# Performance work log

Hardware: AMD Instinct MI355X
Metric: run time of the kernel (lower is better)

## Reference

```python
import jax, jax.numpy as jnp
import numpy as np

N_, E_, A_, B_, H_, DH_ = 8000, 12000, 48000, 64, 64, 4096
STEPS, POOL_ITERS = 4, 3

def rbf(x, K, cutoff):
    mu = jnp.linspace(0.0, cutoff, K).astype(x.dtype)
    gamma = 1.0 / (cutoff / (K - 1)) ** 2
    return jnp.exp(-gamma * (x[..., None] - mu) ** 2)

def gru_step(x, h, Wih, Whh, bih, bhh):
    gi = x @ Wih.T + bih
    gh = h @ Whh.T + bhh
    ir, iz, inew = jnp.split(gi, 3, axis=-1)
    hr, hz, hnew = jnp.split(gh, 3, axis=-1)
    r = jax.nn.sigmoid(ir + hr)
    z = jax.nn.sigmoid(iz + hz)
    n = jnp.tanh(inew + r * hnew)
    return (1.0 - z) * n + z * h

def lstm_step(x, h, c, Wih, Whh, bih, bhh):
    g = x @ Wih.T + bih + h @ Whh.T + bhh
    i, f, gg, o = jnp.split(g, 4, axis=-1)
    c2 = jax.nn.sigmoid(f) * c + jax.nn.sigmoid(i) * jnp.tanh(gg)
    h2 = jax.nn.sigmoid(o) * jnp.tanh(c2)
    return h2, c2

def seg_softmax(e, seg, num_seg):
    m = jax.ops.segment_max(e, seg, num_segments=num_seg)
    ex = jnp.exp(e - m[seg])
    s = jax.ops.segment_sum(ex, seg, num_segments=num_seg)
    return ex / s[seg]

def _forward(node_attribute, edge_attribute, edge_length, angle, edge_src, edge_dst, angle_src, angle_dst, graph_ids, projW, projb, bondW, bondb, efW, efb, gnn_b, buW, bub, auW, aub, gWih, gWhh, gbih, gbhh, sWih0, sWhh0, sbih0, sbhh0, sWih1, sWhh1, sbih1, sbhh1, spW, spb, prelu_a):
    N, E = node_attribute.shape[0], edge_src.shape[0]
    x0 = jax.nn.relu(node_attribute @ projW + projb)  # [N, H]
    len_rbf = rbf(edge_length, 8, 4.0)                # [E, 8]
    edge_feat = jnp.concatenate([edge_attribute, len_rbf], axis=-1)  # [E, 16]
    ee_feat = jnp.concatenate([rbf(angle, 8, float(np.pi)), len_rbf[angle_src]], axis=-1)  # [A, 16]
    Wb = (edge_feat @ bondW + bondb).reshape(E, H_, H_)  # per-bond weight matrices (constant over steps)
    Wa = (ee_feat @ efW + efb).reshape(-1, H_, H_)       # per-angle weight matrices
    nf, hid = x0, x0
    for _ in range(STEPS):
        bm = nf[edge_src]                                # gather src node feats per bond [E, H]
        ha = jax.nn.relu(bm @ auW + aub)                 # angle_update
        m_ang = jnp.einsum('ai,aio->ao', ha[angle_src], Wa)  # [A, H]
        amsg = jax.ops.segment_sum(m_ang, angle_dst, num_segments=E)  # scatter-sum to bonds
        hb = jax.nn.relu(bm @ buW + bub) + amsg          # bond_update + angle message
        m = jnp.einsum('ei,eio->eo', hb, Wb)             # [E, H]
        nf = jax.nn.relu(jax.ops.segment_sum(m, edge_dst, num_segments=N) + gnn_b)
        nf = gru_step(nf, hid, gWih, gWhh, gbih, gbhh)   # 1-step, 1-layer GRU: output == new hidden
        hid = nf
    agg = jnp.concatenate([nf, x0], axis=-1)             # [N, 2H]
    D = agg.shape[-1]
    q_star = jnp.zeros((B_, 2 * D), agg.dtype)
    h0 = jnp.zeros((B_, D), agg.dtype); c0 = h0
    h1 = h0; c1 = h0
    for _ in range(POOL_ITERS):                          # Set2Set
        h0, c0 = lstm_step(q_star, h0, c0, sWih0, sWhh0, sbih0, sbhh0)
        h1, c1 = lstm_step(h0, h1, c1, sWih1, sWhh1, sbih1, sbhh1)
        q = h1                                           # [B, D]
        e = jnp.sum(agg * q[graph_ids], axis=-1)         # [N]
        alpha = seg_softmax(e, graph_ids, B_)
        readout = jax.ops.segment_sum(alpha[:, None] * agg, graph_ids, num_segments=B_)
        q_star = jnp.concatenate([q, readout], axis=-1)  # [B, 2D]
    out = q_star @ spW + spb                             # [B, DH]
    return jnp.where(out >= 0, out, prelu_a * out)       # PReLU

def setup_inputs():
    key = jax.random.key(0)
    ks = jax.random.split(key, 40)
    r = lambda i, shape, s=1.0: s * jax.random.normal(ks[i], shape, jnp.float32)
    inp = {}
    inp['node_attribute'] = r(0, (N_, 110))
    inp['edge_attribute'] = r(1, (E_, 8))
    inp['edge_length'] = jax.random.uniform(ks[2], (E_,), jnp.float32, 0.5, 4.0)
    inp['angle'] = jax.random.uniform(ks[3], (A_,), jnp.float32, 0.0, float(np.pi))
    inp['edge_src'] = jax.random.randint(ks[4], (E_,), 0, N_)
    inp['edge_dst'] = jax.random.randint(ks[5], (E_,), 0, N_)
    inp['angle_src'] = jax.random.randint(ks[6], (A_,), 0, E_)
    inp['angle_dst'] = jax.random.randint(ks[7], (A_,), 0, E_)
    inp['graph_ids'] = jnp.sort(jax.random.randint(ks[8], (N_,), 0, B_))
    w = 0.05
    inp['projW'] = r(9, (110, H_), w); inp['projb'] = jnp.zeros((H_,), jnp.float32)
    inp['bondW'] = r(10, (16, H_ * H_), w); inp['bondb'] = jnp.zeros((H_ * H_,), jnp.float32)
    inp['efW'] = r(11, (16, H_ * H_), w); inp['efb'] = jnp.zeros((H_ * H_,), jnp.float32)
    inp['gnn_b'] = jnp.zeros((H_,), jnp.float32)
    inp['buW'] = r(12, (H_, H_), w); inp['bub'] = jnp.zeros((H_,), jnp.float32)
    inp['auW'] = r(13, (H_, H_), w); inp['aub'] = jnp.zeros((H_,), jnp.float32)
    inp['gWih'] = r(14, (3 * H_, H_), w); inp['gWhh'] = r(15, (3 * H_, H_), w)
    inp['gbih'] = jnp.zeros((3 * H_,), jnp.float32); inp['gbhh'] = jnp.zeros((3 * H_,), jnp.float32)
    D = 2 * H_  # Set2Set feature dim = 128
    inp['sWih0'] = r(16, (4 * D, 2 * D), w); inp['sWhh0'] = r(17, (4 * D, D), w)
    inp['sbih0'] = jnp.zeros((4 * D,), jnp.float32); inp['sbhh0'] = jnp.zeros((4 * D,), jnp.float32)
    inp['sWih1'] = r(18, (4 * D, D), w); inp['sWhh1'] = r(19, (4 * D, D), w)
    inp['sbih1'] = jnp.zeros((4 * D,), jnp.float32); inp['sbhh1'] = jnp.zeros((4 * D,), jnp.float32)
    inp['spW'] = r(20, (4 * H_, DH_), w); inp['spb'] = jnp.zeros((DH_,), jnp.float32)
    inp['prelu_a'] = jnp.full((1,), 0.25, jnp.float32)
    return inp

def reference(node_attribute, edge_attribute, edge_length, angle, edge_src, edge_dst, angle_src, angle_dst, graph_ids, projW, projb, bondW, bondb, efW, efb, gnn_b, buW, bub, auW, aub, gWih, gWhh, gbih, gbhh, sWih0, sWhh0, sbih0, sbhh0, sWih1, sWhh1, sbih1, sbhh1, spW, spb, prelu_a):
    return _forward(node_attribute, edge_attribute, edge_length, angle, edge_src, edge_dst, angle_src, angle_dst, graph_ids, projW, projb, bondW, bondb, efW, efb, gnn_b, buW, bub, auW, aub, gWih, gWhh, gbih, gbhh, sWih0, sWhh0, sbih0, sbhh0, sWih1, sWhh1, sbih1, sbhh1, spW, spb, prelu_a)
```

## Files before the change

kernel.cpp:

```cpp
#include <hip/hip_runtime.h>
#include <math.h>

#define N_N 8000
#define N_E 12000
#define N_A 48000
#define N_B 64
#define N_H 64
#define N_DH 4096

typedef _Float16 h16;
typedef __attribute__((ext_vector_type(8))) _Float16 h16x8;
typedef __attribute__((ext_vector_type(4))) float f32x4;

__device__ __forceinline__ float atomAddF(float* p, float v) {
  return __hip_atomic_fetch_add(p, v, __ATOMIC_RELAXED, __HIP_MEMORY_SCOPE_AGENT);
}
__device__ __forceinline__ float sigm(float x) { return 1.f / (1.f + expf(-x)); }

#define SB_PROJ 2000
#define SB_FEAT (SB_PROJ + 47)
#define SB_PREP (SB_FEAT + 1984)
#define SB_BND  (SB_PREP + 32)
#define SB_END  (SB_BND + 1250)
#define PREP_B0 32768
#define PREP_B1 (PREP_B0 + 69632)
#define PREP_B2 (PREP_B1 + 69632)
#define PREP_B3 (PREP_B2 + 4096)
#define PREP_B4 (PREP_B3 + 4096)
#define PREP_B5 (PREP_B4 + 131072)
#define PREP_B6 (PREP_B5 + 65536)
#define PREP_B7 (PREP_B6 + 65536)
#define PREP_B8 (PREP_B7 + 65536)

__global__ __launch_bounds__(256) void k_setup(
    const float* __restrict__ na, const float* __restrict__ projW,
    const float* __restrict__ projb, const float* __restrict__ ea,
    const float* __restrict__ el, const int* __restrict__ gid,
    const float* __restrict__ gWih, const float* __restrict__ gWhh,
    const float* __restrict__ efW, const float* __restrict__ efb,
    const float* __restrict__ bondW, const float* __restrict__ bondb,
    const float* __restrict__ auW, const float* __restrict__ buW,
    const float* __restrict__ sWih0, const float* __restrict__ sWhh0,
    const float* __restrict__ sWih1, const float* __restrict__ sWhh1,
    float* __restrict__ x0, float* __restrict__ ef,
    int* __restrict__ gstart, int* __restrict__ gend,
    h16* __restrict__ W3t, h16* __restrict__ ttA, h16* __restrict__ ttB,
    h16* __restrict__ wtAU, h16* __restrict__ wtBU,
    float* __restrict__ w0xT, float* __restrict__ w0hT,
    float* __restrict__ w1xT, float* __restrict__ w1hT,
    float4* __restrict__ amsg0_4, float4* __restrict__ nacc0_4) {
  int bx = blockIdx.x, tid = threadIdx.x;
  if (bx < SB_PROJ) {
    int wid = bx * 4 + (tid >> 6);
    int lane = tid & 63;
    if (wid < N_N) {
      const float* row = na + (size_t)wid * 110;
      float acc = projb[lane];
      for (int k = 0; k < 110; ++k) acc = fmaf(row[k], projW[k * 64 + lane], acc);
      x0[(size_t)wid * 64 + lane] = fmaxf(acc, 0.f);
    }
  } else if (bx < SB_FEAT) {
    int e = (bx - SB_PROJ) * 256 + tid;
    if (e < N_E) {
      const float g2 = (7.f / 4.f) * (7.f / 4.f);
      float x = el[e];
#pragma unroll
      for (int j = 0; j < 8; ++j) ef[e * 16 + j] = ea[e * 8 + j];
#pragma unroll
      for (int j = 0; j < 8; ++j) {
        float d = x - j * (4.f / 7.f);
        ef[e * 16 + 8 + j] = expf(-g2 * d * d);
      }
    }
  } else if (bx < SB_PREP) {
    int i = (bx - SB_FEAT) * 256 + tid;
    if (i < PREP_B0) {
      int col = i >> 7, k = i & 127;
      int grp = col >> 6, u = col & 63;
      float v;
      if (grp == 0) v = (k < 64) ? gWih[u * 64 + k] : gWhh[u * 64 + k - 64];
      else if (grp == 1) v = (k < 64) ? gWih[(64 + u) * 64 + k] : gWhh[(64 + u) * 64 + k - 64];
      else if (grp == 2) v = (k < 64) ? gWih[(128 + u) * 64 + k] : 0.f;
      else v = (k < 64) ? 0.f : gWhh[(128 + u) * 64 + k - 64];
      W3t[i] = (h16)v;
    } else if (i < PREP_B1) {
      int j = i - PREP_B0;
      int n = j >> 6, i2 = j & 63;
      int k = n >> 6, o = n & 63;
      float val = (k < 16) ? efW[(size_t)k * 4096 + i2 * 64 + o] : efb[i2 * 64 + o];
      ttA[j] = (h16)val;
    } else if (i < PREP_B2) {
      int j = i - PREP_B1;
      int n = j >> 6, i2 = j & 63;
      int k = n >> 6, o = n & 63;
      float val = (k < 16) ? bondW[(size_t)k * 4096 + i2 * 64 + o] : bondb[i2 * 64 + o];
      ttB[j] = (h16)val;
    } else if (i < PREP_B3) {
      int j = i - PREP_B2;
      int o = j >> 6, i2 = j & 63;
      wtAU[j] = (h16)auW[i2 * 64 + o];
    } else if (i < PREP_B4) {
      int j = i - PREP_B3;
      int o = j >> 6, i2 = j & 63;
      wtBU[j] = (h16)buW[i2 * 64 + o];
    } else if (i < PREP_B5) {
      int j = i - PREP_B4;
      int k = j >> 9, r = j & 511;
      w0xT[j] = sWih0[(size_t)r * 256 + k];
    } else if (i < PREP_B6) {
      int j = i - PREP_B5;
      int k = j >> 9, r = j & 511;
      w0hT[j] = sWhh0[(size_t)r * 128 + k];
    } else if (i < PREP_B7) {
      int j = i - PREP_B6;
      int k = j >> 9, r = j & 511;
      w1xT[j] = sWih1[(size_t)r * 128 + k];
    } else if (i < PREP_B8) {
      int j = i - PREP_B7;
      int k = j >> 9, r = j & 511;
      w1hT[j] = sWhh1[(size_t)r * 128 + k];
    }
  } else if (bx < SB_BND) {
    int n = (bx - SB_PREP) * 256 + tid;
    if (n < N_N) {
      int g = gid[n];
      if (n == 0 || gid[n - 1] != g) gstart[g] = n;
      if (n == N_N - 1 || gid[n + 1] != g) gend[g] = n + 1;
    }
  } else if (bx < SB_END) {
    int i = (bx - SB_BND) * 256 + tid;
    float4 z = (float4){0.f, 0.f, 0.f, 0.f};
    if (i < 192000) amsg0_4[i] = z;
    else if (i < 320000) nacc0_4[i - 192000] = z;
  }
}

__global__ __launch_bounds__(256) void k_edgeP(
    const float* __restrict__ xcur, const int* __restrict__ esrc,
    const h16* __restrict__ wtAU, const float* __restrict__ aub,
    const h16* __restrict__ ttA, const float* __restrict__ ef,
    h16* __restrict__ P8, float* __restrict__ Q) {
  __shared__ h16 haT[4][2048];
  __shared__ float f_lds[128 * 9];
  int tid = threadIdx.x, wave = tid >> 6, lane = tid & 63;
  int l15 = lane & 15, lq = lane >> 4;
  int oc = blockIdx.y;
  int base = blockIdx.x * 128;
  if (oc >= 2) {
    for (int e2 = tid; e2 < 128 * 8; e2 += 256) {
      int il = e2 >> 3, k = e2 & 7;
      int g = base + il;
      if (g >= N_E) g = N_E - 1;
      f_lds[il * 9 + k] = ef[(size_t)g * 16 + 8 + k];
    }
    __syncthreads();
  }
  int ibl = wave * 32, ib0 = base + ibl;
  h16* myT = haT[wave];

  {
    h16x8 xafr[2][2];
#pragma unroll
    for (int s = 0; s < 2; ++s) {
      int item = ib0 + s * 16 + l15;
      if (item >= N_E) item = N_E - 1;
      const float* vp = xcur + (size_t)esrc[item] * 64;
#pragma unroll
      for (int ks = 0; ks < 2; ++ks) {
        const float4* p = (const float4*)(vp + ks * 32 + 8 * lq);
        float4 v0 = p[0], v1 = p[1];
        h16x8 a;
        a[0] = (h16)v0.x; a[1] = (h16)v0.y; a[2] = (h16)v0.z; a[3] = (h16)v0.w;
        a[4] = (h16)v1.x; a[5] = (h16)v1.y; a[6] = (h16)v1.z; a[7] = (h16)v1.w;
        xafr[s][ks] = a;
      }
    }
    f32x4 aU[2][4];
#pragma unroll
    for (int s = 0; s < 2; ++s)
#pragma unroll
      for (int nt = 0; nt < 4; ++nt) aU[s][nt] = (f32x4){0.f, 0.f, 0.f, 0.f};
#pragma unroll
    for (int nt = 0; nt < 4; ++nt)
#pragma unroll
      for (int ks = 0; ks < 2; ++ks) {
        h16x8 b = *(const h16x8*)(wtAU + (size_t)(nt * 16 + l15) * 64 + ks * 32 + 8 * lq);
#pragma unroll
        for (int s = 0; s < 2; ++s)
          aU[s][nt] = __builtin_amdgcn_mfma_f32_16x16x32_f16(xafr[s][ks], b, aU[s][nt], 0, 0, 0);
      }
#pragma unroll
    for (int s = 0; s < 2; ++s)
#pragma unroll
      for (int nt = 0; nt < 4; ++nt) {
        int o = nt * 16 + l15;
        float bo = aub[o];
#pragma unroll
        for (int r = 0; r < 4; ++r) {
          int row = s * 16 + lq * 4 + r;
          float val = fmaxf(aU[s][nt][r] + bo, 0.f);
          int idx = (((row * 64 + o) << 1) ^ ((row & 7) << 4)) >> 1;
          myT[idx] = (h16)val;
        }
      }
  }
  h16x8 afr[2][2];
#pragma unroll
  for (int s = 0; s < 2; ++s)
#pragma unroll
    for (int ks = 0; ks < 2; ++ks) {
      int row = s * 16 + l15;
      int byte = ((row * 64 + ks * 32 + 8 * lq) << 1) ^ ((row & 7) << 4);
      afr[s][ks] = *(const h16x8*)((const char*)myT + byte);
    }

  if (oc < 2) {
#pragma unroll
    for (int kk = oc * 4; kk < oc * 4 + 4; ++kk) {
      f32x4 acc[2][4];
#pragma unroll
      for (int s = 0; s < 2; ++s)
#pragma unroll
        for (int nt = 0; nt < 4; ++nt) acc[s][nt] = (f32x4){0.f, 0.f, 0.f, 0.f};
#pragma unroll
      for (int nt = 0; nt < 4; ++nt)
#pragma unroll
        for (int ks = 0; ks < 2; ++ks) {
          h16x8 b = *(const h16x8*)(ttA + (size_t)(kk * 64 + nt * 16 + l15) * 64 +
                                    ks * 32 + 8 * lq);
#pragma unroll
          for (int s = 0; s < 2; ++s)
            acc[s][nt] = __builtin_amdgcn_mfma_f32_16x16x32_f16(afr[s][ks], b, acc[s][nt], 0, 0, 0);
        }
#pragma unroll
      for (int s = 0; s < 2; ++s)
#pragma unroll
        for (int r = 0; r < 4; ++r) {
          int e = ib0 + s * 16 + lq * 4 + r;
          if (e < N_E) {
#pragma unroll
            for (int nt = 0; nt < 4; ++nt)
              P8[((size_t)e * 8 + kk) * 64 + nt * 16 + l15] = (h16)acc[s][nt][r];
          }
        }
    }
  } else {
    int no = oc - 2;
    f32x4 qacc[2][2];
#pragma unroll
    for (int s = 0; s < 2; ++s)
#pragma unroll
      for (int nt = 0; nt < 2; ++nt) qacc[s][nt] = (f32x4){0.f, 0.f, 0.f, 0.f};
    for (int kk = 8; kk < 16; ++kk) {
      h16x8 a2[2][2];
#pragma unroll
      for (int s = 0; s < 2; ++s) {
        h16 fs = (h16)f_lds[(ibl + s * 16 + l15) * 9 + (kk - 8)];
        a2[s][0] = afr[s][0] * fs;
        a2[s][1] = afr[s][1] * fs;
      }
#pragma unroll
      for (int nt = 0; nt < 2; ++nt)
#pragma unroll
        for (int ks = 0; ks < 2; ++ks) {
          h16x8 b = *(const h16x8*)(ttA + (size_t)(kk * 64 + (no * 2 + nt) * 16 + l15) * 64 +
                                    ks * 32 + 8 * lq);
#pragma unroll
          for (int s = 0; s < 2; ++s)
            qacc[s][nt] = __builtin_amdgcn_mfma_f32_16x16x32_f16(a2[s][ks], b, qacc[s][nt], 0, 0, 0);
        }
    }
#pragma unroll
    for (int nt = 0; nt < 2; ++nt)
#pragma unroll
      for (int ks = 0; ks < 2; ++ks) {
        h16x8 b = *(const h16x8*)(ttA + (size_t)(16 * 64 + (no * 2 + nt) * 16 + l15) * 64 +
                                  ks * 32 + 8 * lq);
#pragma unroll
        for (int s = 0; s < 2; ++s)
          qacc[s][nt] = __builtin_amdgcn_mfma_f32_16x16x32_f16(afr[s][ks], b, qacc[s][nt], 0, 0, 0);
      }
#pragma unroll
    for (int s = 0; s < 2; ++s)
#pragma unroll
      for (int r = 0; r < 4; ++r) {
        int e = ib0 + s * 16 + lq * 4 + r;
        if (e < N_E) {
#pragma unroll
          for (int nt = 0; nt < 2; ++nt)
            Q[(size_t)e * 64 + (no * 2 + nt) * 16 + l15] = qacc[s][nt][r];
        }
      }
  }
}

__global__ __launch_bounds__(256) void k_angle(
    const float* __restrict__ ang, const int* __restrict__ asrc,
    const int* __restrict__ adst, const h16* __restrict__ P8,
    const float* __restrict__ Q, float* __restrict__ amsg) {
  int w = (blockIdx.x * blockDim.x + threadIdx.x) >> 6;
  int lane = threadIdx.x & 63;
  if (w >= N_A) return;
  float x = ang[w];
  int e = asrc[w], d = adst[w];
  float acc = Q[(size_t)e * 64 + lane];
  const h16* p = P8 + (size_t)e * 512;
  const float PIf = 3.14159265358979323846f;
  const float g1 = (7.f / PIf) * (7.f / PIf);
#pragma unroll
  for (int j = 0; j < 8; ++j) {
    float dd = x - j * (PIf / 7.f);
    acc = fmaf(expf(-g1 * dd * dd), (float)p[j * 64 + lane], acc);
  }
  atomAddF(amsg + (size_t)d * 64 + lane, acc);
}

__global__ __launch_bounds__(256) void k_bond(
    const float* __restrict__ xcur, const int* __restrict__ esrc,
    const h16* __restrict__ wtBU, const float* __restrict__ bub,
    const float* __restrict__ amsg_in, const float* __restrict__ ef,
    const h16* __restrict__ ttB, const int* __restrict__ edst,
    float* __restrict__ nacc, float4* __restrict__ zbuf, int zcount4) {
  if (blockIdx.y == 0) {
    int stride = gridDim.x * 256;
    for (int i = blockIdx.x * 256 + threadIdx.x; i < zcount4; i += stride)
      zbuf[i] = (float4){0.f, 0.f, 0.f, 0.f};
  }
  __shared__ h16 haT[4][2048];
  __shared__ float f_lds[128 * 17];
  __shared__ int dst_lds[128];
  int tid = threadIdx.x;
  int base = blockIdx.x * 128;
  int oc = blockIdx.y;
  for (int e2 = tid; e2 < 128 * 16; e2 += 256) {
    int il = e2 >> 4, k = e2 & 15;
    int g = base + il;
    if (g >= N_E) g = N_E - 1;
    f_lds[il * 17 + k] = ef[(size_t)g * 16 + k];
  }
  if (tid < 128) {
    int g = base + tid;
    if (g >= N_E) g = N_E - 1;
    dst_lds[tid] = edst[g];
  }
  __syncthreads();

  int wave = tid >> 6, lane = tid & 63;
  int l15 = lane & 15, lq = lane >> 4;
  int ibl = wave * 32, ib0 = base + ibl;
  h16* myT = haT[wave];

  {
    h16x8 xafr[2][2];
#pragma unroll
    for (int s = 0; s < 2; ++s) {
      int item = ib0 + s * 16 + l15;
      if (item >= N_E) item = N_E - 1;
      const float* vp = xcur + (size_t)esrc[item] * 64;
#pragma unroll
      for (int ks = 0; ks < 2; ++ks) {
        const float4* p = (const float4*)(vp + ks * 32 + 8 * lq);
        float4 v0 = p[0], v1 = p[1];
        h16x8 a;
        a[0] = (h16)v0.x; a[1] = (h16)v0.y; a[2] = (h16)v0.z; a[3] = (h16)v0.w;
        a[4] = (h16)v1.x; a[5] = (h16)v1.y; a[6] = (h16)v1.z; a[7] = (h16)v1.w;
        xafr[s][ks] = a;
      }
    }
    f32x4 aU[2][4];
#pragma unroll
    for (int s = 0; s < 2; ++s)
#pragma unroll
      for (int nt = 0; nt < 4; ++nt) aU[s][nt] = (f32x4){0.f, 0.f, 0.f, 0.f};
#pragma unroll
    for (int nt = 0; nt < 4; ++nt)
#pragma unroll
      for (int ks = 0; ks < 2; ++ks) {
        h16x8 b = *(const h16x8*)(wtBU + (size_t)(nt * 16 + l15) * 64 + ks * 32 + 8 * lq);
#pragma unroll
        for (int s = 0; s < 2; ++s)
          aU[s][nt] = __builtin_amdgcn_mfma_f32_16x16x32_f16(xafr[s][ks], b, aU[s][nt], 0, 0, 0);
      }
#pragma unroll
    for (int s = 0; s < 2; ++s)
#pragma unroll
      for (int nt = 0; nt < 4; ++nt) {
        int o = nt * 16 + l15;
        float bo = bub[o];
#pragma unroll
        for (int r = 0; r < 4; ++r) {
          int row = s * 16 + lq * 4 + r;
          int item = ib0 + row;
          if (item >= N_E) item = N_E - 1;
          float val = fmaxf(aU[s][nt][r] + bo, 0.f) + amsg_in[(size_t)item * 64 + o];
          int idx = (((row * 64 + o) << 1) ^ ((row & 7) << 4)) >> 1;
          myT[idx] = (h16)val;
        }
      }
  }
  h16x8 afr[2][2];
#pragma unroll
  for (int s = 0; s < 2; ++s)
#pragma unroll
    for (int ks = 0; ks < 2; ++ks) {
      int row = s * 16 + l15;
      int byte = ((row * 64 + ks * 32 + 8 * lq) << 1) ^ ((row & 7) << 4);
      afr[s][ks] = *(const h16x8*)((const char*)myT + byte);
    }

  f32x4 acc[2];
  acc[0] = (f32x4){0.f, 0.f, 0.f, 0.f};
  acc[1] = (f32x4){0.f, 0.f, 0.f, 0.f};
  for (int kk = 0; kk < 16; ++kk) {
    h16x8 bfr[2];
#pragma unroll
    for (int ks = 0; ks < 2; ++ks)
      bfr[ks] = *(const h16x8*)(ttB + (size_t)(kk * 64 + oc * 16 + l15) * 64 + ks * 32 + 8 * lq);
    h16x8 a2[2][2];
#pragma unroll
    for (int s = 0; s < 2; ++s) {
      h16 fs = (h16)f_lds[(ibl + s * 16 + l15) * 17 + kk];
      a2[s][0] = afr[s][0] * fs;
      a2[s][1] = afr[s][1] * fs;
    }
#pragma unroll
    for (int s = 0; s < 2; ++s)
#pragma unroll
      for (int ks = 0; ks < 2; ++ks)
        acc[s] = __builtin_amdgcn_mfma_f32_16x16x32_f16(a2[s][ks], bfr[ks], acc[s], 0, 0, 0);
  }
  {
    h16x8 bfr[2];
#pragma unroll
    for (int ks = 0; ks < 2; ++ks)
      bfr[ks] = *(const h16x8*)(ttB + (size_t)(16 * 64 + oc * 16 + l15) * 64 + ks * 32 + 8 * lq);
#pragma unroll
    for (int s = 0; s < 2; ++s)
#pragma unroll
      for (int ks = 0; ks < 2; ++ks)
        acc[s] = __builtin_amdgcn_mfma_f32_16x16x32_f16(afr[s][ks], bfr[ks], acc[s], 0, 0, 0);
  }
#pragma unroll
  for (int s = 0; s < 2; ++s)
#pragma unroll
    for (int r = 0; r < 4; ++r) {
      int il = ibl + s * 16 + lq * 4 + r;
      int item = base + il;
      if (item < N_E)
        atomAddF(nacc + (size_t)dst_lds[il] * 64 + oc * 16 + l15, acc[s][r]);
    }
}

__global__ __launch_bounds__(256) void k_gru2(
    const float* __restrict__ nacc, const float* __restrict__ gnnb,
    const float* __restrict__ h, const h16* __restrict__ W3t,
    const float* __restrict__ gbih, const float* __restrict__ gbhh,
    float* __restrict__ hout, const float* __restrict__ x0,
    float* __restrict__ agg, int wagg, float4* __restrict__ zbuf, int zcount4) {
  if (zbuf) {
    int stride = gridDim.x * 256;
    for (int i = blockIdx.x * 256 + threadIdx.x; i < zcount4; i += stride)
      zbuf[i] = (float4){0.f, 0.f, 0.f, 0.f};
  }
  int tid = threadIdx.x, wave = tid >> 6, lane = tid & 63;
  int l15 = lane & 15, lq = lane >> 4;
  int ib0 = blockIdx.x * 64 + wave * 16;
  int nodeA = ib0 + l15;
  if (nodeA >= N_N) nodeA = N_N - 1;

  h16x8 afr[4];
#pragma unroll
  for (int ks = 0; ks < 2; ++ks) {
    const float4* p = (const float4*)(nacc + (size_t)nodeA * 64 + ks * 32 + 8 * lq);
    const float4* gp = (const float4*)(gnnb + ks * 32 + 8 * lq);
    float4 v0 = p[0], v1 = p[1], g0 = gp[0], g1 = gp[1];
    h16x8 a;
    a[0] = (h16)fmaxf(v0.x + g0.x, 0.f); a[1] = (h16)fmaxf(v0.y + g0.y, 0.f);
    a[2] = (h16)fmaxf(v0.z + g0.z, 0.f); a[3] = (h16)fmaxf(v0.w + g0.w, 0.f);
    a[4] = (h16)fmaxf(v1.x + g1.x, 0.f); a[5] = (h16)fmaxf(v1.y + g1.y, 0.f);
    a[6] = (h16)fmaxf(v1.z + g1.z, 0.f); a[7] = (h16)fmaxf(v1.w + g1.w, 0.f);
    afr[ks] = a;
  }
#pragma unroll
  for (int ks = 0; ks < 2; ++ks) {
    const float4* p = (const float4*)(h + (size_t)nodeA * 64 + ks * 32 + 8 * lq);
    float4 v0 = p[0], v1 = p[1];
    h16x8 a;
    a[0] = (h16)v0.x; a[1] = (h16)v0.y; a[2] = (h16)v0.z; a[3] = (h16)v0.w;
    a[4] = (h16)v1.x; a[5] = (h16)v1.y; a[6] = (h16)v1.z; a[7] = (h16)v1.w;
    afr[2 + ks] = a;
  }

  f32x4 acc[16];
#pragma unroll
  for (int nt = 0; nt < 16; ++nt) acc[nt] = (f32x4){0.f, 0.f, 0.f, 0.f};
#pragma unroll
  for (int nt = 0; nt < 16; ++nt) {
#pragma unroll
    for (int ks = 0; ks < 4; ++ks) {
      if (nt >= 8 && nt < 12 && ks >= 2) continue;
      if (nt >= 12 && ks < 2) continue;
      h16x8 b = *(const h16x8*)(W3t + (size_t)(nt * 16 + l15) * 128 + ks * 32 + 8 * lq);
      acc[nt] = __builtin_amdgcn_mfma_f32_16x16x32_f16(afr[ks], b, acc[nt], 0, 0, 0);
    }
  }

#pragma unroll
  for (int nt0 = 0; nt0 < 4; ++nt0) {
    int u = nt0 * 16 + l15;
    float br = gbih[u] + gbhh[u];
    float bz = gbih[64 + u] + gbhh[64 + u];
    float bin_ = gbih[128 + u];
    float bhn = gbhh[128 + u];
#pragma unroll
    for (int r = 0; r < 4; ++r) {
      int node = ib0 + lq * 4 + r;
      if (node < N_N) {
        float rr = sigm(acc[nt0][r] + br);
        float zz = sigm(acc[nt0 + 4][r] + bz);
        float nn = tanhf(acc[nt0 + 8][r] + bin_ + rr * (acc[nt0 + 12][r] + bhn));
        float hv = h[(size_t)node * 64 + u];
        float val = (1.f - zz) * nn + zz * hv;
        hout[(size_t)node * 64 + u] = val;
        if (wagg) {
          agg[(size_t)node * 128 + u] = val;
          agg[(size_t)node * 128 + 64 + u] = x0[(size_t)node * 64 + u];
        }
      }
    }
  }
}

__global__ __launch_bounds__(256) void k_s2s(
    const float* __restrict__ agg, const int* __restrict__ gstart,
    const int* __restrict__ gend,
    const float* __restrict__ w0xT, const float* __restrict__ w0hT,
    const float* __restrict__ sbih0, const float* __restrict__ sbhh0,
    const float* __restrict__ w1xT, const float* __restrict__ w1hT,
    const float* __restrict__ sbih1, const float* __restrict__ sbhh1,
    const float* __restrict__ spW, const float* __restrict__ spb,
    const float* __restrict__ pa, float* __restrict__ out) {
  int g = blockIdx.x, tid = threadIdx.x;
  __shared__ float qs[256];
  __shared__ float h0[128], c0[128], h1[128], c1[128];
  __shared__ float gates[512];
  __shared__ float ew[1024];
  __shared__ float red[8];
  __shared__ float comb[256];
  if (tid < 256) qs[tid] = 0.f;
  if (tid < 128) { h0[tid] = 0.f; c0[tid] = 0.f; h1[tid] = 0.f; c1[tid] = 0.f; }
  int s = gstart[g], t = gend[g];
  int cnt = t - s;
  if (cnt < 0) cnt = 0;
  if (cnt > 1024) cnt = 1024;
  int wave = tid >> 6, lane = tid & 63;
  __syncthreads();

  for (int it = 0; it < 3; ++it) {
    {
      int r0 = tid, r1 = tid + 256;
      float a0 = sbih0[r0] + sbhh0[r0];
      float a1 = sbih0[r1] + sbhh0[r1];
      for (int k = 0; k < 256; ++k) {
        float xv = qs[k];
        a0 = fmaf(xv, w0xT[(size_t)k * 512 + r0], a0);
        a1 = fmaf(xv, w0xT[(size_t)k * 512 + r1], a1);
      }
      for (int k = 0; k < 128; ++k) {
        float hv = h0[k];
        a0 = fmaf(hv, w0hT[(size_t)k * 512 + r0], a0);
        a1 = fmaf(hv, w0hT[(size_t)k * 512 + r1], a1);
      }
      gates[r0] = a0;
      gates[r1] = a1;
    }
    __syncthreads();
    if (tid < 128) {
      float gi = gates[tid], gf = gates[128 + tid], gg = gates[256 + tid], go = gates[384 + tid];
      float c2 = sigm(gf) * c0[tid] + sigm(gi) * tanhf(gg);
      c0[tid] = c2;
      h0[tid] = sigm(go) * tanhf(c2);
    }
    __syncthreads();
    {
      int r0 = tid, r1 = tid + 256;
      float a0 = sbih1[r0] + sbhh1[r0];
      float a1 = sbih1[r1] + sbhh1[r1];
      for (int k = 0; k < 128; ++k) {
        float xv = h0[k], hv = h1[k];
        a0 = fmaf(xv, w1xT[(size_t)k * 512 + r0], a0);
        a1 = fmaf(xv, w1xT[(size_t)k * 512 + r1], a1);
        a0 = fmaf(hv, w1hT[(size_t)k * 512 + r0], a0);
        a1 = fmaf(hv, w1hT[(size_t)k * 512 + r1], a1);
      }
      gates[r0] = a0;
      gates[r1] = a1;
    }
    __syncthreads();
    if (tid < 128) {
      float gi = gates[tid], gf = gates[128 + tid], gg = gates[256 + tid], go = gates[384 + tid];
      float c2 = sigm(gf) * c1[tid] + sigm(gi) * tanhf(gg);
      c1[tid] = c2;
      h1[tid] = sigm(go) * tanhf(c2);
    }
    __syncthreads();
    for (int i = wave; i < cnt; i += 4) {
      int n = s + i;
      float a = agg[(size_t)n * 128 + lane] * h1[lane] +
                agg[(size_t)n * 128 + 64 + lane] * h1[64 + lane];
#pragma unroll
      for (int m = 1; m < 64; m <<= 1) a += __shfl_xor(a, m);
      if (lane == 0) ew[i] = a;
    }
    __syncthreads();
    float mx = -INFINITY;
    for (int i = tid; i < cnt; i += 256) mx = fmaxf(mx, ew[i]);
#pragma unroll
    for (int m = 1; m < 64; m <<= 1) mx = fmaxf(mx, __shfl_xor(mx, m));
    if (lane == 0) red[wave] = mx;
    __syncthreads();
    mx = fmaxf(fmaxf(red[0], red[1]), fmaxf(red[2], red[3]));
    float sm = 0.f;
    for (int i = tid; i < cnt; i += 256) sm += expf(ew[i] - mx);
#pragma unroll
    for (int m = 1; m < 64; m <<= 1) sm += __shfl_xor(sm, m);
    if (lane == 0) red[4 + wave] = sm;
    __syncthreads();
    sm = red[4] + red[5] + red[6] + red[7];
    float inv = (sm > 0.f) ? 1.f / sm : 0.f;
    __syncthreads();
    for (int i = tid; i < cnt; i += 256) ew[i] = expf(ew[i] - mx) * inv;
    __syncthreads();
    int d = tid & 127, half = tid >> 7;
    float acc = 0.f;
    for (int i = half; i < cnt; i += 2)
      acc = fmaf(ew[i], agg[(size_t)(s + i) * 128 + d], acc);
    comb[tid] = acc;
    __syncthreads();
    if (half == 0) {
      qs[d] = h1[d];
      qs[128 + d] = acc + comb[128 + tid];
    }
    __syncthreads();
  }
  float a_ = pa[0];
  float oacc[16];
#pragma unroll
  for (int j = 0; j < 16; ++j) oacc[j] = spb[j * 256 + tid];
  for (int k = 0; k < 256; ++k) {
    float qv = qs[k];
    const float* wr = spW + (size_t)k * 4096;
#pragma unroll
    for (int j = 0; j < 16; ++j) oacc[j] = fmaf(qv, wr[j * 256 + tid], oacc[j]);
  }
#pragma unroll
  for (int j = 0; j < 16; ++j) {
    float v = oacc[j];
    out[(size_t)g * 4096 + j * 256 + tid] = v >= 0.f ? v : a_ * v;
  }
}

enum : size_t {
  OFF_X0 = 0,
  OFF_HA = OFF_X0 + (size_t)N_N * 64,
  OFF_HB = OFF_HA + (size_t)N_N * 64,
  OFF_EF = OFF_HB + (size_t)N_N * 64,
  OFF_AMSG0 = OFF_EF + (size_t)N_E * 16,
  OFF_AMSG1 = OFF_AMSG0 + (size_t)N_E * 64,
  OFF_NACC0 = OFF_AMSG1 + (size_t)N_E * 64,
  OFF_NACC1 = OFF_NACC0 + (size_t)N_N * 64,
  OFF_AGG = OFF_NACC1 + (size_t)N_N * 64,
  OFF_GSTART = OFF_AGG + (size_t)N_N * 128,
  OFF_GEND = OFF_GSTART + N_B,
  OFF_TT_ANG = (OFF_GEND + N_B + 63) & ~(size_t)63,
  OFF_TT_BOND = OFF_TT_ANG + 34816,
  OFF_WT_AU = OFF_TT_BOND + 34816,
  OFF_WT_BU = OFF_WT_AU + 2048,
  OFF_W3T = OFF_WT_BU + 2048,
  OFF_P8 = OFF_W3T + 16384,
  OFF_Q = OFF_P8 + 3072000,
  OFF_W0XT = OFF_Q + 768000,
  OFF_W0HT = OFF_W0XT + 131072,
  OFF_W1XT = OFF_W0HT + 65536,
  OFF_W1HT = OFF_W1XT + 65536,
  WS_FLOATS = OFF_W1HT + 65536
};

extern "C" void kernel_launch(void* const* d_in, const int* in_sizes, int n_in,
                              void* d_out, int out_size, void* d_ws, size_t ws_size,
                              hipStream_t stream) {
  (void)in_sizes; (void)n_in; (void)out_size; (void)ws_size;
  const float* na    = (const float*)d_in[0];
  const float* ea    = (const float*)d_in[1];
  const float* el    = (const float*)d_in[2];
  const float* ang   = (const float*)d_in[3];
  const int*   esrc  = (const int*)d_in[4];
  const int*   edst  = (const int*)d_in[5];
  const int*   asrc  = (const int*)d_in[6];
  const int*   adst  = (const int*)d_in[7];
  const int*   gid   = (const int*)d_in[8];
  const float* projW = (const float*)d_in[9];
  const float* projb = (const float*)d_in[10];
  const float* bondW = (const float*)d_in[11];
  const float* bondb = (const float*)d_in[12];
  const float* efW   = (const float*)d_in[13];
  const float* efb   = (const float*)d_in[14];
  const float* gnnb  = (const float*)d_in[15];
  const float* buW   = (const float*)d_in[16];
  const float* bub   = (const float*)d_in[17];
  const float* auW   = (const float*)d_in[18];
  const float* aub   = (const float*)d_in[19];
  const float* gWih  = (const float*)d_in[20];
  const float* gWhh  = (const float*)d_in[21];
  const float* gbih  = (const float*)d_in[22];
  const float* gbhh  = (const float*)d_in[23];
  const float* sWih0 = (const float*)d_in[24];
  const float* sWhh0 = (const float*)d_in[25];
  const float* sbih0 = (const float*)d_in[26];
  const float* sbhh0 = (const float*)d_in[27];
  const float* sWih1 = (const float*)d_in[28];
  const float* sWhh1 = (const float*)d_in[29];
  const float* sbih1 = (const float*)d_in[30];
  const float* sbhh1 = (const float*)d_in[31];
  const float* spW   = (const float*)d_in[32];
  const float* spb   = (const float*)d_in[33];
  const float* pa    = (const float*)d_in[34];
  float* out = (float*)d_out;
  float* ws = (float*)d_ws;

  float* x0    = ws + OFF_X0;
  float* hA    = ws + OFF_HA;
  float* hB    = ws + OFF_HB;
  float* ef    = ws + OFF_EF;
  float* amsg0 = ws + OFF_AMSG0;
  float* amsg1 = ws + OFF_AMSG1;
  float* nacc0 = ws + OFF_NACC0;
  float* nacc1 = ws + OFF_NACC1;
  float* agg   = ws + OFF_AGG;
  int* gstart  = (int*)(ws + OFF_GSTART);
  h16* ttA  = (h16*)(ws + OFF_TT_ANG);
  h16* ttB  = (h16*)(ws + OFF_TT_BOND);
  h16* wtAU = (h16*)(ws + OFF_WT_AU);
  h16* wtBU = (h16*)(ws + OFF_WT_BU);
  h16* w3t  = (h16*)(ws + OFF_W3T);
  h16* P8   = (h16*)(ws + OFF_P8);
  float* Q    = ws + OFF_Q;
  float* w0xT = ws + OFF_W0XT;
  float* w0hT = ws + OFF_W0HT;
  float* w1xT = ws + OFF_W1XT;
  float* w1hT = ws + OFF_W1HT;

  hipMemsetAsync(gstart, 0x7f, 2 * N_B * sizeof(int), stream);
  k_setup<<<SB_END, 256, 0, stream>>>(
      na, projW, projb, ea, el, gid, gWih, gWhh, efW, efb, bondW, bondb, auW, buW,
      sWih0, sWhh0, sWih1, sWhh1, x0, ef, gstart, gstart + N_B, w3t, ttA, ttB,
      wtAU, wtBU, w0xT, w0hT, w1xT, w1hT, (float4*)amsg0, (float4*)nacc0);

  const int EGX = (N_E + 127) / 128;
  const float* cur = x0;
  float* bufs[2] = {hA, hB};
  float* amsgs[2] = {amsg0, amsg1};
  float* naccs[2] = {nacc0, nacc1};
  for (int s = 0; s < 4; ++s) {
    float* amsg_c = amsgs[s & 1];
    float* amsg_o = amsgs[(s + 1) & 1];
    float* nacc_c = naccs[s & 1];
    float* nacc_o = naccs[(s + 1) & 1];
    k_edgeP<<<dim3(EGX, 4), 256, 0, stream>>>(cur, esrc, wtAU, aub, ttA, ef, P8, Q);
    k_angle<<<(N_A * 64) / 256, 256, 0, stream>>>(ang, asrc, adst, P8, Q, amsg_c);
    k_bond<<<dim3(EGX, 4), 256, 0, stream>>>(cur, esrc, wtBU, bub, amsg_c, ef, ttB,
                                             edst, nacc_c, (float4*)amsg_o,
                                             N_E * 64 / 4);
    float* nxt = bufs[s & 1];
    k_gru2<<<(N_N + 63) / 64, 256, 0, stream>>>(nacc_c, gnnb, cur, w3t, gbih, gbhh,
                                                nxt, x0, agg, (s == 3) ? 1 : 0,
                                                (float4*)nacc_o, N_N * 64 / 4);
    cur = nxt;
  }

  k_s2s<<<N_B, 256, 0, stream>>>(agg, gstart, gstart + N_B, w0xT, w0hT, sbih0, sbhh0,
                                 w1xT, w1hT, sbih1, sbhh1, spW, spb, pa, out);
}
```

Measured before the change: 442.1 us.

## Split Set2Set pooling into parallel LSTM, pooling and output kernels

Replaces the single per-graph Set2Set kernel, which ran only 64 blocks, with a sequence of smaller kernels. The LSTM matvecs use one wave per (graph, unit) with shuffle reductions over the original weight layout. Attention pooling keeps one block per graph, and the final 256×4096 projection runs as a fully parallel kernel instead of 64 blocks each streaming the whole weight matrix. The setup kernel no longer builds transposed LSTM weights; it now zeroes the new q*/h/c state buffers. The goal is to remove the serial, low-occupancy tail, at the cost of about ten extra kernel launches and round-trips of state through global memory.

```diff
diff --git a/kernel.cpp b/kernel.cpp
--- a/kernel.cpp
+++ b/kernel.cpp
@@ -19,18 +19,14 @@
 
 #define SB_PROJ 2000
 #define SB_FEAT (SB_PROJ + 47)
-#define SB_PREP (SB_FEAT + 1984)
+#define SB_PREP (SB_FEAT + 704)
 #define SB_BND  (SB_PREP + 32)
-#define SB_END  (SB_BND + 1250)
+#define SB_END  (SB_BND + 1330)
 #define PREP_B0 32768
 #define PREP_B1 (PREP_B0 + 69632)
 #define PREP_B2 (PREP_B1 + 69632)
 #define PREP_B3 (PREP_B2 + 4096)
 #define PREP_B4 (PREP_B3 + 4096)
-#define PREP_B5 (PREP_B4 + 131072)
-#define PREP_B6 (PREP_B5 + 65536)
-#define PREP_B7 (PREP_B6 + 65536)
-#define PREP_B8 (PREP_B7 + 65536)
 
 __global__ __launch_bounds__(256) void k_setup(
     const float* __restrict__ na, const float* __restrict__ projW,
@@ -40,15 +36,12 @@
     const float* __restrict__ efW, const float* __restrict__ efb,
     const float* __restrict__ bondW, const float* __restrict__ bondb,
     const float* __restrict__ auW, const float* __restrict__ buW,
-    const float* __restrict__ sWih0, const float* __restrict__ sWhh0,
-    const float* __restrict__ sWih1, const float* __restrict__ sWhh1,
     float* __restrict__ x0, float* __restrict__ ef,
     int* __restrict__ gstart, int* __restrict__ gend,
     h16* __restrict__ W3t, h16* __restrict__ ttA, h16* __restrict__ ttB,
     h16* __restrict__ wtAU, h16* __restrict__ wtBU,
-    float* __restrict__ w0xT, float* __restrict__ w0hT,
-    float* __restrict__ w1xT, float* __restrict__ w1hT,
-    float4* __restrict__ amsg0_4, float4* __restrict__ nacc0_4) {
+    float4* __restrict__ amsg0_4, float4* __restrict__ nacc0_4,
+    float4* __restrict__ qz_4) {
   int bx = blockIdx.x, tid = threadIdx.x;
   if (bx < SB_PROJ) {
     int wid = bx * 4 + (tid >> 6);
@@ -103,22 +96,6 @@
       int j = i - PREP_B3;
       int o = j >> 6, i2 = j & 63;
       wtBU[j] = (h16)buW[i2 * 64 + o];
-    } else if (i < PREP_B5) {
-      int j = i - PREP_B4;
-      int k = j >> 9, r = j & 511;
-      w0xT[j] = sWih0[(size_t)r * 256 + k];
-    } else if (i < PREP_B6) {
-      int j = i - PREP_B5;
-      int k = j >> 9, r = j & 511;
-      w0hT[j] = sWhh0[(size_t)r * 128 + k];
-    } else if (i < PREP_B7) {
-      int j = i - PREP_B6;
-      int k = j >> 9, r = j & 511;
-      w1xT[j] = sWih1[(size_t)r * 128 + k];
-    } else if (i < PREP_B8) {
-      int j = i - PREP_B7;
-      int k = j >> 9, r = j & 511;
-      w1hT[j] = sWhh1[(size_t)r * 128 + k];
     }
   } else if (bx < SB_BND) {
     int n = (bx - SB_PREP) * 256 + tid;
@@ -132,6 +109,7 @@
     float4 z = (float4){0.f, 0.f, 0.f, 0.f};
     if (i < 192000) amsg0_4[i] = z;
     else if (i < 320000) nacc0_4[i - 192000] = z;
+    else if (i < 340480) qz_4[i - 320000] = z;
   }
 }
 
@@ -531,133 +509,118 @@
   }
 }
 
-__global__ __launch_bounds__(256) void k_s2s(
+
+__global__ __launch_bounds__(256) void k_lstm2(
+    const float* __restrict__ x, int xdim,
+    const float* __restrict__ hin, const float* __restrict__ cin,
+    const float* __restrict__ Wih, const float* __restrict__ Whh,
+    const float* __restrict__ bih, const float* __restrict__ bhh,
+    float* __restrict__ hout, float* __restrict__ cout) {
+  int w = (blockIdx.x * blockDim.x + threadIdx.x) >> 6;
+  int lane = threadIdx.x & 63;
+  if (w >= N_B * 128) return;
+  int b = w >> 7, u = w & 127;
+  float a0 = 0.f, a1 = 0.f, a2 = 0.f, a3 = 0.f;
+  const float* xr = x + (size_t)b * xdim;
+  for (int k = lane; k < xdim; k += 64) {
+    float xv = xr[k];
+    a0 = fmaf(xv, Wih[(size_t)u * xdim + k], a0);
+    a1 = fmaf(xv, Wih[(size_t)(128 + u) * xdim + k], a1);
+    a2 = fmaf(xv, Wih[(size_t)(256 + u) * xdim + k], a2);
+    a3 = fmaf(xv, Wih[(size_t)(384 + u) * xdim + k], a3);
+  }
+  const float* hr = hin + (size_t)b * 128;
+#pragma unroll
+  for (int k0 = 0; k0 < 128; k0 += 64) {
+    int k = k0 + lane;
+    float hv = hr[k];
+    a0 = fmaf(hv, Whh[(size_t)u * 128 + k], a0);
+    a1 = fmaf(hv, Whh[(size_t)(128 + u) * 128 + k], a1);
+    a2 = fmaf(hv, Whh[(size_t)(256 + u) * 128 + k], a2);
+    a3 = fmaf(hv, Whh[(size_t)(384 + u) * 128 + k], a3);
+  }
+#pragma unroll
+  for (int m = 1; m < 64; m <<= 1) {
+    a0 += __shfl_xor(a0, m);
+    a1 += __shfl_xor(a1, m);
+    a2 += __shfl_xor(a2, m);
+    a3 += __shfl_xor(a3, m);
+  }
+  if (lane == 0) {
+    float gi = a0 + bih[u] + bhh[u];
+    float gf = a1 + bih[128 + u] + bhh[128 + u];
+    float gg = a2 + bih[256 + u] + bhh[256 + u];
+    float go = a3 + bih[384 + u] + bhh[384 + u];
+    float c2 = sigm(gf) * cin[(size_t)b * 128 + u] + sigm(gi) * tanhf(gg);
+    hout[(size_t)b * 128 + u] = sigm(go) * tanhf(c2);
+    cout[(size_t)b * 128 + u] = c2;
+  }
+}
+
+__global__ __launch_bounds__(256) void k_pool2(
     const float* __restrict__ agg, const int* __restrict__ gstart,
-    const int* __restrict__ gend,
-    const float* __restrict__ w0xT, const float* __restrict__ w0hT,
-    const float* __restrict__ sbih0, const float* __restrict__ sbhh0,
-    const float* __restrict__ w1xT, const float* __restrict__ w1hT,
-    const float* __restrict__ sbih1, const float* __restrict__ sbhh1,
-    const float* __restrict__ spW, const float* __restrict__ spb,
-    const float* __restrict__ pa, float* __restrict__ out) {
-  int g = blockIdx.x, tid = threadIdx.x;
-  __shared__ float qs[256];
-  __shared__ float h0[128], c0[128], h1[128], c1[128];
-  __shared__ float gates[512];
-  __shared__ float ew[1024];
-  __shared__ float red[8];
-  __shared__ float comb[256];
-  if (tid < 256) qs[tid] = 0.f;
-  if (tid < 128) { h0[tid] = 0.f; c0[tid] = 0.f; h1[tid] = 0.f; c1[tid] = 0.f; }
+    const int* __restrict__ gend, const float* __restrict__ q,
+    float* __restrict__ q_star) {
+  int g = blockIdx.x;
   int s = gstart[g], t = gend[g];
   int cnt = t - s;
   if (cnt < 0) cnt = 0;
   if (cnt > 1024) cnt = 1024;
-  int wave = tid >> 6, lane = tid & 63;
+  __shared__ float ew[1024];
+  __shared__ float red[8];
+  __shared__ float comb[256];
+  int tid = threadIdx.x, wave = tid >> 6, lane = tid & 63;
+  float qa = q[g * 128 + lane], qb = q[g * 128 + 64 + lane];
+  for (int i = wave; i < cnt; i += 4) {
+    int n = s + i;
+    float a = agg[(size_t)n * 128 + lane] * qa + agg[(size_t)n * 128 + 64 + lane] * qb;
+#pragma unroll
+    for (int m = 1; m < 64; m <<= 1) a += __shfl_xor(a, m);
+    if (lane == 0) ew[i] = a;
+  }
   __syncthreads();
-
-  for (int it = 0; it < 3; ++it) {
-    {
-      int r0 = tid, r1 = tid + 256;
-      float a0 = sbih0[r0] + sbhh0[r0];
-      float a1 = sbih0[r1] + sbhh0[r1];
-      for (int k = 0; k < 256; ++k) {
-        float xv = qs[k];
-        a0 = fmaf(xv, w0xT[(size_t)k * 512 + r0], a0);
-        a1 = fmaf(xv, w0xT[(size_t)k * 512 + r1], a1);
-      }
-      for (int k = 0; k < 128; ++k) {
-        float hv = h0[k];
-        a0 = fmaf(hv, w0hT[(size_t)k * 512 + r0], a0);
-        a1 = fmaf(hv, w0hT[(size_t)k * 512 + r1], a1);
-      }
-      gates[r0] = a0;
-      gates[r1] = a1;
-    }
-    __syncthreads();
-    if (tid < 128) {
-      float gi = gates[tid], gf = gates[128 + tid], gg = gates[256 + tid], go = gates[384 + tid];
-      float c2 = sigm(gf) * c0[tid] + sigm(gi) * tanhf(gg);
-      c0[tid] = c2;
-      h0[tid] = sigm(go) * tanhf(c2);
-    }
-    __syncthreads();
-    {
-      int r0 = tid, r1 = tid + 256;
-      float a0 = sbih1[r0] + sbhh1[r0];
-      float a1 = sbih1[r1] + sbhh1[r1];
-      for (int k = 0; k < 128; ++k) {
-        float xv = h0[k], hv = h1[k];
-        a0 = fmaf(xv, w1xT[(size_t)k * 512 + r0], a0);
-        a1 = fmaf(xv, w1xT[(size_t)k * 512 + r1], a1);
-        a0 = fmaf(hv, w1hT[(size_t)k * 512 + r0], a0);
-        a1 = fmaf(hv, w1hT[(size_t)k * 512 + r1], a1);
-      }
-      gates[r0] = a0;
-      gates[r1] = a1;
-    }
-    __syncthreads();
-    if (tid < 128) {
-      float gi = gates[tid], gf = gates[128 + tid], gg = gates[256 + tid], go = gates[384 + tid];
-      float c2 = sigm(gf) * c1[tid] + sigm(gi) * tanhf(gg);
-      c1[tid] = c2;
-      h1[tid] = sigm(go) * tanhf(c2);
-    }
-    __syncthreads();
-    for (int i = wave; i < cnt; i += 4) {
-      int n = s + i;
-      float a = agg[(size_t)n * 128 + lane] * h1[lane] +
-                agg[(size_t)n * 128 + 64 + lane] * h1[64 + lane];
-#pragma unroll
-      for (int m = 1; m < 64; m <<= 1) a += __shfl_xor(a, m);
-      if (lane == 0) ew[i] = a;
-    }
-    __syncthreads();
-    float mx = -INFINITY;
-    for (int i = tid; i < cnt; i += 256) mx = fmaxf(mx, ew[i]);
-#pragma unroll
-    for (int m = 1; m < 64; m <<= 1) mx = fmaxf(mx, __shfl_xor(mx, m));
-    if (lane == 0) red[wave] = mx;
-    __syncthreads();
-    mx = fmaxf(fmaxf(red[0], red[1]), fmaxf(red[2], red[3]));
-    float sm = 0.f;
-    for (int i = tid; i < cnt; i += 256) sm += expf(ew[i] - mx);
-#pragma unroll
-    for (int m = 1; m < 64; m <<= 1) sm += __shfl_xor(sm, m);
-    if (lane == 0) red[4 + wave] = sm;
-    __syncthreads();
-    sm = red[4] + red[5] + red[6] + red[7];
-    float inv = (sm > 0.f) ? 1.f / sm : 0.f;
-    __syncthreads();
-    for (int i = tid; i < cnt; i += 256) ew[i] = expf(ew[i] - mx) * inv;
-    __syncthreads();
-    int d = tid & 127, half = tid >> 7;
-    float acc = 0.f;
-    for (int i = half; i < cnt; i += 2)
-      acc = fmaf(ew[i], agg[(size_t)(s + i) * 128 + d], acc);
-    comb[tid] = acc;
-    __syncthreads();
-    if (half == 0) {
-      qs[d] = h1[d];
-      qs[128 + d] = acc + comb[128 + tid];
-    }
-    __syncthreads();
-  }
-  float a_ = pa[0];
-  float oacc[16];
-#pragma unroll
-  for (int j = 0; j < 16; ++j) oacc[j] = spb[j * 256 + tid];
-  for (int k = 0; k < 256; ++k) {
-    float qv = qs[k];
-    const float* wr = spW + (size_t)k * 4096;
-#pragma unroll
-    for (int j = 0; j < 16; ++j) oacc[j] = fmaf(qv, wr[j * 256 + tid], oacc[j]);
-  }
-#pragma unroll
-  for (int j = 0; j < 16; ++j) {
-    float v = oacc[j];
-    out[(size_t)g * 4096 + j * 256 + tid] = v >= 0.f ? v : a_ * v;
-  }
+  float mx = -INFINITY;
+  for (int i = tid; i < cnt; i += 256) mx = fmaxf(mx, ew[i]);
+#pragma unroll
+  for (int m = 1; m < 64; m <<= 1) mx = fmaxf(mx, __shfl_xor(mx, m));
+  if (lane == 0) red[wave] = mx;
+  __syncthreads();
+  mx = fmaxf(fmaxf(red[0], red[1]), fmaxf(red[2], red[3]));
+  float sm = 0.f;
+  for (int i = tid; i < cnt; i += 256) sm += expf(ew[i] - mx);
+#pragma unroll
+  for (int m = 1; m < 64; m <<= 1) sm += __shfl_xor(sm, m);
+  if (lane == 0) red[4 + wave] = sm;
+  __syncthreads();
+  sm = red[4] + red[5] + red[6] + red[7];
+  float inv = (sm > 0.f) ? 1.f / sm : 0.f;
+  __syncthreads();
+  for (int i = tid; i < cnt; i += 256) ew[i] = expf(ew[i] - mx) * inv;
+  __syncthreads();
+  int d = tid & 127, half = tid >> 7;
+  float acc = 0.f;
+  for (int i = half; i < cnt; i += 2)
+    acc = fmaf(ew[i], agg[(size_t)(s + i) * 128 + d], acc);
+  comb[tid] = acc;
+  __syncthreads();
+  if (half == 0) {
+    float r2 = acc + comb[128 + tid];
+    q_star[(size_t)g * 256 + d] = q[(size_t)g * 128 + d];
+    q_star[(size_t)g * 256 + 128 + d] = r2;
+  }
+}
+
+__global__ void k_out(const float* __restrict__ qs, const float* __restrict__ W,
+                      const float* __restrict__ bias, const float* __restrict__ pa,
+                      float* __restrict__ out) {
+  int idx = blockIdx.x * blockDim.x + threadIdx.x;
+  if (idx >= N_B * N_DH) return;
+  int b = idx >> 12, d = idx & 4095;
+  float acc = bias[d];
+  const float* q = qs + (size_t)b * 256;
+  for (int k = 0; k < 256; ++k) acc = fmaf(q[k], W[(size_t)k * 4096 + d], acc);
+  float a = pa[0];
+  out[idx] = acc >= 0.f ? acc : a * acc;
 }
 
 enum : size_t {
@@ -670,7 +633,16 @@
   OFF_NACC0 = OFF_AMSG1 + (size_t)N_E * 64,
   OFF_NACC1 = OFF_NACC0 + (size_t)N_N * 64,
   OFF_AGG = OFF_NACC1 + (size_t)N_N * 64,
-  OFF_GSTART = OFF_AGG + (size_t)N_N * 128,
+  OFF_QSTAR = OFF_AGG + (size_t)N_N * 128,
+  OFF_H0A = OFF_QSTAR + N_B * 256,
+  OFF_H0B = OFF_H0A + N_B * 128,
+  OFF_C0A = OFF_H0B + N_B * 128,
+  OFF_C0B = OFF_C0A + N_B * 128,
+  OFF_H1A = OFF_C0B + N_B * 128,
+  OFF_H1B = OFF_H1A + N_B * 128,
+  OFF_C1A = OFF_H1B + N_B * 128,
+  OFF_C1B = OFF_C1A + N_B * 128,
+  OFF_GSTART = OFF_C1B + N_B * 128,
   OFF_GEND = OFF_GSTART + N_B,
   OFF_TT_ANG = (OFF_GEND + N_B + 63) & ~(size_t)63,
   OFF_TT_BOND = OFF_TT_ANG + 34816,
@@ -679,11 +651,7 @@
   OFF_W3T = OFF_WT_BU + 2048,
   OFF_P8 = OFF_W3T + 16384,
   OFF_Q = OFF_P8 + 3072000,
-  OFF_W0XT = OFF_Q + 768000,
-  OFF_W0HT = OFF_W0XT + 131072,
-  OFF_W1XT = OFF_W0HT + 65536,
-  OFF_W1HT = OFF_W1XT + 65536,
-  WS_FLOATS = OFF_W1HT + 65536
+  WS_FLOATS = OFF_Q + 768000
 };
 
 extern "C" void kernel_launch(void* const* d_in, const int* in_sizes, int n_in,
@@ -737,6 +705,11 @@
   float* nacc0 = ws + OFF_NACC0;
   float* nacc1 = ws + OFF_NACC1;
   float* agg   = ws + OFF_AGG;
+  float* qstar = ws + OFF_QSTAR;
+  float* h0a = ws + OFF_H0A; float* h0b = ws + OFF_H0B;
+  float* c0a = ws + OFF_C0A; float* c0b = ws + OFF_C0B;
+  float* h1a = ws + OFF_H1A; float* h1b = ws + OFF_H1B;
+  float* c1a = ws + OFF_C1A; float* c1b = ws + OFF_C1B;
   int* gstart  = (int*)(ws + OFF_GSTART);
   h16* ttA  = (h16*)(ws + OFF_TT_ANG);
   h16* ttB  = (h16*)(ws + OFF_TT_BOND);
@@ -745,16 +718,12 @@
   h16* w3t  = (h16*)(ws + OFF_W3T);
   h16* P8   = (h16*)(ws + OFF_P8);
   float* Q    = ws + OFF_Q;
-  float* w0xT = ws + OFF_W0XT;
-  float* w0hT = ws + OFF_W0HT;
-  float* w1xT = ws + OFF_W1XT;
-  float* w1hT = ws + OFF_W1HT;
 
   hipMemsetAsync(gstart, 0x7f, 2 * N_B * sizeof(int), stream);
   k_setup<<<SB_END, 256, 0, stream>>>(
       na, projW, projb, ea, el, gid, gWih, gWhh, efW, efb, bondW, bondb, auW, buW,
-      sWih0, sWhh0, sWih1, sWhh1, x0, ef, gstart, gstart + N_B, w3t, ttA, ttB,
-      wtAU, wtBU, w0xT, w0hT, w1xT, w1hT, (float4*)amsg0, (float4*)nacc0);
+      x0, ef, gstart, gstart + N_B, w3t, ttA, ttB, wtAU, wtBU,
+      (float4*)amsg0, (float4*)nacc0, (float4*)qstar);
 
   const int EGX = (N_E + 127) / 128;
   const float* cur = x0;
@@ -778,6 +747,19 @@
     cur = nxt;
   }
 
-  k_s2s<<<N_B, 256, 0, stream>>>(agg, gstart, gstart + N_B, w0xT, w0hT, sbih0, sbhh0,
-                                 w1xT, w1hT, sbih1, sbhh1, spW, spb, pa, out);
-}
+  float *h0i = h0a, *h0o = h0b, *c0i = c0a, *c0o = c0b;
+  float *h1i = h1a, *h1o = h1b, *c1i = c1a, *c1o = c1b;
+  for (int it = 0; it < 3; ++it) {
+    k_lstm2<<<(N_B * 128 * 64 + 255) / 256, 256, 0, stream>>>(
+        qstar, 256, h0i, c0i, sWih0, sWhh0, sbih0, sbhh0, h0o, c0o);
+    k_lstm2<<<(N_B * 128 * 64 + 255) / 256, 256, 0, stream>>>(
+        h0o, 128, h1i, c1i, sWih1, sWhh1, sbih1, sbhh1, h1o, c1o);
+    k_pool2<<<N_B, 256, 0, stream>>>(agg, gstart, gstart + N_B, h1o, qstar);
+    float* tmp;
+    tmp = h0i; h0i = h0o; h0o = tmp;
+    tmp = c0i; c0i = c0o; c0o = tmp;
+    tmp = h1i; h1i = h1o; h1o = tmp;
+    tmp = c1i; c1i = c1o; c1o = tmp;
+  }
+  k_out<<<(N_B * N_DH + 255) / 256, 256, 0, stream>>>(qstar, spW, spb, pa, out);
+}
```

Result: faster. 395.5 us (-10.5%).
